# Optimization experiments

Hardware: AMD Instinct MI355X
Metric: run time of the kernel (lower is better)

## Reference

```python
import jax, jax.numpy as jnp
import numpy as np

B, L, C, P, H, DK, MRD = 16, 1024, 512, 64, 8, 64, 7
STD = 0.02


def _layernorm(x, g, b):
    mu = x.mean(-1, keepdims=True)
    var = ((x - mu) ** 2).mean(-1, keepdims=True)
    return (x - mu) / jnp.sqrt(var + 1e-5) * g + b


def _rel_pos_table(L, m):
    i = jnp.arange(L)
    d = jnp.abs(i[:, None] - i[None, :]).astype(jnp.float32)
    d = jnp.where(d > m, m + jnp.log2(jnp.maximum(d - m, 1.0)), d)
    return jnp.clip(d, 0, 2 * m).astype(jnp.int32)  # (L, L) in [0, 2m]


def setup_inputs() -> dict:
    key = jax.random.key(0)
    ks = jax.random.split(key, 16)
    inp = {
        'qx': jax.random.normal(ks[0], (B, L, C), jnp.float32),
        'kx': jax.random.normal(ks[1], (B, L, C), jnp.float32),
        'vx': jax.random.normal(ks[2], (B, L, C), jnp.float32),
        'maskPAD': jnp.ones((B, L, L), jnp.int32),
        'Wp': jax.random.normal(ks[3], (C, P)) * STD,
        'bp': jnp.zeros((P,)),
        'WQ': jax.random.normal(ks[4], (C, H * DK)) * STD,
        'bQ': jnp.zeros((H * DK,)),
        'WK': jax.random.normal(ks[5], (C, H * DK)) * STD,
        'bK': jnp.zeros((H * DK,)),
        'WV': jax.random.normal(ks[6], (C, H * DK)) * STD,
        'bV': jnp.zeros((H * DK,)),
        'WO': jax.random.normal(ks[7], (H * DK, C)) * STD,
        'bO': jnp.zeros((C,)),
        'embK': jax.random.normal(ks[8], (2 * MRD + 1, H)) * STD,
        'embB': jax.random.normal(ks[9], (2 * MRD + 1, H)) * STD,
        'ln1_g': jnp.ones((C,)), 'ln1_b': jnp.zeros((C,)),
        'ln2_g': jnp.ones((C,)), 'ln2_b': jnp.zeros((C,)),
        'W1': jax.random.normal(ks[10], (C, 4 * C)) * STD,
        'b1': jnp.zeros((4 * C,)),
        'W2': jax.random.normal(ks[11], (4 * C, C)) * STD,
        'b2': jnp.zeros((C,)),
    }
    return inp


def reference(qx, kx, vx, maskPAD, Wp, bp, WQ, bQ, WK, bK, WV, bV, WO, bO,
              embK, embB, ln1_g, ln1_b, ln2_g, ln2_b, W1, b1, W2, b2):
    B_, L_, C_ = qx.shape
    P_ = Wp.shape[1]
    H_ = embK.shape[1]
    DK_ = WV.shape[1] // H_
    m = (embK.shape[0] - 1) // 2

    # pseudo-token attention pooling
    pScore = vx @ Wp + bp                                   # (B, L, P)
    pad = (maskPAD[:, 0] == 0)                              # (B, L)
    pScore = jnp.where(pad[:, :, None], -2.0 ** 15, pScore)
    pAlpha = jax.nn.softmax(pScore, axis=1)                 # softmax over L
    kxp = jnp.einsum('blp,blc->bpc', pAlpha, kx)            # (B, P, C)
    vxp = jnp.einsum('blp,blc->bpc', pAlpha, vx)
    pA = jax.lax.stop_gradient(pAlpha)                      # .detach()

    # multi-head attention vs pseudo tokens
    q = (qx @ WQ + bQ).reshape(B_, L_, H_, DK_).transpose(0, 2, 1, 3)   # (B,H,L,dk)
    k = (kxp @ WK + bK).reshape(B_, P_, H_, DK_).transpose(0, 2, 1, 3)  # (B,H,P,dk)
    v = (vxp @ WV + bV).reshape(B_, P_, H_, DK_).transpose(0, 2, 1, 3)
    scores = jnp.einsum('bhld,bhpd->bhlp', q, k) / np.sqrt(DK_).astype(np.float32)

    # relative position multiplicative/additive bias, pooled through pA
    tab = _rel_pos_table(L_, m)                             # (L, L)
    Krel = embK[tab].transpose(2, 0, 1)                     # (H, L, L)
    brel = embB[tab].transpose(2, 0, 1)
    Kb = jnp.einsum('hlm,bmp->bhlp', Krel, pA)
    bb = jnp.einsum('hlm,bmp->bhlp', brel, pA)
    scores = scores * Kb + bb

    alpha = jax.nn.softmax(scores, axis=3)
    z = jnp.einsum('bhlp,bhpd->bhld', alpha, v)
    z = z.transpose(0, 2, 1, 3).reshape(B_, L_, H_ * DK_)
    z = z @ WO + bO

    # FFN block (residuals against vx, post-LN)
    z1 = _layernorm(vx + z, ln1_g, ln1_b)
    ffn = jax.nn.gelu(z1 @ W1 + b1, approximate=False) @ W2 + b2
    x = _layernorm(z1 + ffn, ln2_g, ln2_b)
    return x
```

## Files before the change

### kernel.cpp

```cpp
#include <hip/hip_runtime.h>
#include <hip/hip_bf16.h>

#define BI   16
#define LSEQ 1024
#define CDIM 512
#define PDIM 64
#define HH   8
#define DKK  64

typedef __hip_bfloat16 bf16;
typedef unsigned short u16;
typedef __attribute__((ext_vector_type(8))) short bf16x8;
typedef __attribute__((ext_vector_type(4))) float f32x4;

__constant__ int c_dlo[15] = {0,1,2,3,4,5,6,7, 9,11,15,23,39, 71,135};
__constant__ int c_dhi[15] = {0,1,2,3,4,5,6,8,10,14,22,38,70,134,1023};

__device__ __forceinline__ float b2f(u16 u) {
    union { unsigned int i; float f; } c; c.i = ((unsigned int)u) << 16; return c.f;
}
__device__ __forceinline__ u16 f2bu(float v) {
    bf16 h = __float2bfloat16(v);
    return *(u16*)&h;
}
__device__ __forceinline__ float ldDyn(const void* p, size_t i, int f) {
    return f ? ((const float*)p)[i] : b2f(((const u16*)p)[i]);
}
__device__ __forceinline__ void ld4Dyn(const void* p, size_t i, int f, float* o) {
    if (f) { float4 v = *(const float4*)((const float*)p + i);
             o[0]=v.x; o[1]=v.y; o[2]=v.z; o[3]=v.w; }
    else   { ushort4 u = *(const ushort4*)((const u16*)p + i);
             o[0]=b2f(u.x); o[1]=b2f(u.y); o[2]=b2f(u.z); o[3]=b2f(u.w); }
}

__device__ __forceinline__ void gll16(const u16* g, u16* l) {
    __builtin_amdgcn_global_load_lds(
        (const __attribute__((address_space(1))) unsigned int*)g,
        (__attribute__((address_space(3))) unsigned int*)l,
        16, 0, 0);
}

__device__ __forceinline__ float wsum(float v) {
    #pragma unroll
    for (int o = 32; o; o >>= 1) v += __shfl_xor(v, o, 64);
    return v;
}
__device__ __forceinline__ float wmax(float v) {
    #pragma unroll
    for (int o = 32; o; o >>= 1) v = fmaxf(v, __shfl_xor(v, o, 64));
    return v;
}

__global__ void k_detect(const unsigned int* __restrict__ qw, int* __restrict__ flag) {
    __shared__ int cnt;
    if (threadIdx.x == 0) cnt = 0;
    __syncthreads();
    int local = 0;
    for (int i = threadIdx.x; i < 4096; i += 256) {
        float fv = b2f((u16)(qw[i] & 0xFFFFu));
        float af = fabsf(fv);
        if (fv == 0.0f || (af >= 0.0009765625f && af <= 32.0f)) local++;
    }
    atomicAdd(&cnt, local);
    __syncthreads();
    if (threadIdx.x == 0) flag[0] = (cnt >= 2048) ? 0 : 1;
}

__global__ __launch_bounds__(256) void k_cvt2(
    const void* __restrict__ s0, u16* __restrict__ d0,
    const void* __restrict__ s1, u16* __restrict__ d1,
    const int* __restrict__ flag, int n)
{
    const int fA = flag[0];
    const void* src = blockIdx.y ? s1 : s0;
    u16* dst = blockIdx.y ? d1 : d0;
    int i = (blockIdx.x * 256 + threadIdx.x) * 4;
    if (i >= n) return;
    float t[4]; ld4Dyn(src, i, fA, t);
    ushort4 o; o.x = f2bu(t[0]); o.y = f2bu(t[1]); o.z = f2bu(t[2]); o.w = f2bu(t[3]);
    *(ushort4*)(dst + i) = o;
}

__device__ __forceinline__ void transp_core(
    const void* W, u16* WT, int fd, int Kd, int Nd, int bx, int by)
{
    __shared__ u16 t[32][33];
    const int tx = threadIdx.x & 31, ty = threadIdx.x >> 5;
    #pragma unroll
    for (int r = 0; r < 32; r += 8) {
        int k = by * 32 + ty + r, n = bx * 32 + tx;
        t[ty + r][tx] = f2bu(ldDyn(W, (size_t)k * Nd + n, fd));
    }
    __syncthreads();
    #pragma unroll
    for (int r = 0; r < 32; r += 8) {
        int n = bx * 32 + ty + r, k = by * 32 + tx;
        WT[(size_t)n * Kd + k] = t[tx][ty + r];
    }
}

__global__ __launch_bounds__(256) void k_transp(
    const void* __restrict__ W, u16* __restrict__ WT, const int* __restrict__ flag,
    int Kd, int Nd)
{
    transp_core(W, WT, flag[0], Kd, Nd, blockIdx.x, blockIdx.y);
}

__global__ __launch_bounds__(256) void k_transp4(
    const void* __restrict__ W0, u16* __restrict__ T0,
    const void* __restrict__ W1, u16* __restrict__ T1,
    const void* __restrict__ W2, u16* __restrict__ T2,
    const void* __restrict__ W3, u16* __restrict__ T3,
    const int* __restrict__ flag)
{
    const void* W; u16* T;
    switch (blockIdx.z) {
        case 0: W = W0; T = T0; break;
        case 1: W = W1; T = T1; break;
        case 2: W = W2; T = T2; break;
        default: W = W3; T = T3; break;
    }
    transp_core(W, T, flag[0], 512, 512, blockIdx.x, blockIdx.y);
}

__global__ __launch_bounds__(256) void k_transpcv(
    const void* __restrict__ kx, const u16* __restrict__ vxb,
    u16* __restrict__ kxT, u16* __restrict__ vxT, const int* __restrict__ flag)
{
    const int t = blockIdx.z >> 4;
    const int b = blockIdx.z & 15;
    const int l0 = blockIdx.x * 64, c0 = blockIdx.y * 32;
    __shared__ u16 s[32][72];
    const int tid = threadIdx.x;
    if (t == 0) {
        const int fd = flag[0];
        #pragma unroll
        for (int p = 0; p < 2; ++p) {
            int l = (tid >> 3) + p * 32, c4 = (tid & 7) * 4;
            float v[4];
            ld4Dyn(kx, ((size_t)b * LSEQ + l0 + l) * CDIM + c0 + c4, fd, v);
            #pragma unroll
            for (int k = 0; k < 4; ++k) s[c4 + k][l] = f2bu(v[k]);
        }
    } else {
        #pragma unroll
        for (int p = 0; p < 2; ++p) {
            int l = (tid >> 3) + p * 32, c4 = (tid & 7) * 4;
            ushort4 u = *(const ushort4*)&vxb[((size_t)b * LSEQ + l0 + l) * CDIM + c0 + c4];
            s[c4 + 0][l] = u.x; s[c4 + 1][l] = u.y;
            s[c4 + 2][l] = u.z; s[c4 + 3][l] = u.w;
        }
    }
    __syncthreads();
    u16* dst = t ? vxT : kxT;
    #pragma unroll
    for (int p = 0; p < 2; ++p) {
        int c = (tid >> 4) + p * 16, l4 = (tid & 15) * 4;
        *(ushort4*)&dst[((size_t)b * CDIM + c0 + c) * LSEQ + l0 + l4] =
            *(const ushort4*)&s[c][l4];
    }
}

__device__ __forceinline__ void gemm_core(
    u16 (*As)[32], u16 (*Bs)[32],
    const u16* A, const u16* BT, const void* bias, const u16* res, void* Cc, int fd,
    int K, int lda, int ldbt, int ldc, size_t bOff, int mode, int outBf, int perm,
    int m0, int n0)
{
    const int tid = threadIdx.x;
    const int wave = tid >> 6, lane = tid & 63;
    const int q = lane >> 4, l16 = lane & 15;
    const int wm = (wave >> 1) * 64, wn = (wave & 1) * 64;
    const int srow = wave * 16 + (lane >> 2);
    const int scol = (lane & 3) * 8;

    f32x4 acc[4][4];
    #pragma unroll
    for (int i = 0; i < 4; ++i)
        #pragma unroll
        for (int j = 0; j < 4; ++j) acc[i][j] = (f32x4){0.f, 0.f, 0.f, 0.f};

    #pragma unroll
    for (int pass = 0; pass < 2; ++pass) {
        int row = pass * 64 + srow;
        gll16(A + (size_t)(m0 + row) * lda + scol, &As[pass * 64 + wave * 16][0]);
        gll16(BT + (size_t)(n0 + row) * ldbt + scol, &Bs[pass * 64 + wave * 16][0]);
    }
    __syncthreads();

    int cur = 0;
    for (int k0 = 0; k0 < K; k0 += 32) {
        if (k0 + 32 < K) {
            const int nb = (cur ^ 1) * 128;
            #pragma unroll
            for (int pass = 0; pass < 2; ++pass) {
                int row = pass * 64 + srow;
                gll16(A + (size_t)(m0 + row) * lda + (k0 + 32) + scol,
                      &As[nb + pass * 64 + wave * 16][0]);
                gll16(BT + (size_t)(n0 + row) * ldbt + (k0 + 32) + scol,
                      &Bs[nb + pass * 64 + wave * 16][0]);
            }
        }
        const int cb = cur * 128;
        bf16x8 af[4], bfr[4];
        #pragma unroll
        for (int i = 0; i < 4; ++i) af[i] = *(const bf16x8*)&As[cb + wm + i * 16 + l16][q * 8];
        #pragma unroll
        for (int j = 0; j < 4; ++j) bfr[j] = *(const bf16x8*)&Bs[cb + wn + j * 16 + l16][q * 8];
        #pragma unroll
        for (int i = 0; i < 4; ++i)
            #pragma unroll
            for (int j = 0; j < 4; ++j)
                acc[i][j] = __builtin_amdgcn_mfma_f32_16x16x32_bf16(af[i], bfr[j], acc[i][j], 0, 0, 0);
        __syncthreads();
        cur ^= 1;
    }

    #pragma unroll
    for (int i = 0; i < 4; ++i) {
        int row = m0 + wm + i * 16 + q * 4;
        #pragma unroll
        for (int j = 0; j < 4; ++j) {
            int col = n0 + wn + j * 16 + l16;
            #pragma unroll
            for (int r = 0; r < 4; ++r) {
                float v = acc[i][j][r];
                int m = row + r;
                if (mode == 2) {
                    v += ldDyn(bias, bOff + col, fd) + b2f(res[(size_t)m * ldc + col]);
                    ((float*)Cc)[(size_t)m * ldc + col] = v;
                } else {
                    v += ldDyn(bias, bOff + col, fd);
                    if (mode == 1) v = 0.5f * v * (1.0f + erff(v * 0.70710678118654752f));
                    size_t idx = perm ? (size_t)((m >> 6) << 15) + ((size_t)col << 6) + (m & 63)
                                      : (size_t)m * ldc + col;
                    if (outBf) ((u16*)Cc)[idx] = f2bu(v);
                    else       ((float*)Cc)[idx] = v;
                }
            }
        }
    }
}

__global__ __launch_bounds__(256) void gemm_mfma(
    const u16* __restrict__ A, const u16* __restrict__ BT, const void* __restrict__ bias,
    const u16* __restrict__ res, void* __restrict__ Cc, const int* __restrict__ flag,
    int K, int lda, int ldbt, int ldc, size_t bOff, int mode, int outBf, int perm)
{
    __shared__ u16 As[256][32];
    __shared__ u16 Bs[256][32];
    gemm_core(As, Bs, A, BT, bias, res, Cc, flag[0], K, lda, ldbt, ldc, bOff,
              mode, outBf, perm, blockIdx.y * 128, blockIdx.x * 128);
}

__global__ __launch_bounds__(256) void gemm_kv(
    const u16* __restrict__ A0, const u16* __restrict__ A1,
    const u16* __restrict__ BT0, const u16* __restrict__ BT1,
    const void* __restrict__ b0, const void* __restrict__ b1,
    void* __restrict__ C0, void* __restrict__ C1, const int* __restrict__ flag)
{
    __shared__ u16 As[256][32];
    __shared__ u16 Bs[256][32];
    const int z = blockIdx.z;
    gemm_core(As, Bs, z ? A1 : A0, z ? BT1 : BT0, z ? b1 : b0, nullptr,
              z ? C1 : C0, flag[0],
              CDIM, CDIM, CDIM, CDIM, 0, 0, 1, z ? 1 : 0,
              blockIdx.y * 128, blockIdx.x * 128);
}

__global__ __launch_bounds__(256) void gemm_pool(
    const u16* __restrict__ pAT, const u16* __restrict__ kxT,
    const u16* __restrict__ vxT, u16* __restrict__ kvxb)
{
    __shared__ u16 As[128][32];
    __shared__ u16 Bs[256][32];
    const int b = blockIdx.y;
    const int n0 = blockIdx.x * 128;
    const u16* Ag = pAT + (size_t)b * (PDIM * LSEQ);
    const u16* Bg = (blockIdx.z ? vxT : kxT) + (size_t)b * (CDIM * LSEQ);
    u16* Cg = kvxb + (size_t)blockIdx.z * 524288 + (size_t)b * (PDIM * CDIM);

    const int tid = threadIdx.x;
    const int wave = tid >> 6, lane = tid & 63;
    const int q = lane >> 4, l16 = lane & 15;
    const int wm = (wave >> 1) * 32, wn = (wave & 1) * 64;
    const int srow = lane >> 2, scol = (lane & 3) * 8;

    f32x4 acc[2][4];
    #pragma unroll
    for (int i = 0; i < 2; ++i)
        #pragma unroll
        for (int j = 0; j < 4; ++j) acc[i][j] = (f32x4){0.f, 0.f, 0.f, 0.f};

    gll16(Ag + (size_t)(wave * 16 + srow) * LSEQ + scol, &As[wave * 16][0]);
    #pragma unroll
    for (int pass = 0; pass < 2; ++pass)
        gll16(Bg + (size_t)(n0 + wave * 32 + pass * 16 + srow) * LSEQ + scol,
              &Bs[wave * 32 + pass * 16][0]);
    __syncthreads();

    int cur = 0;
    for (int k0 = 0; k0 < LSEQ; k0 += 32) {
        if (k0 + 32 < LSEQ) {
            const int na = (cur ^ 1) * 64, nb = (cur ^ 1) * 128;
            gll16(Ag + (size_t)(wave * 16 + srow) * LSEQ + (k0 + 32) + scol,
                  &As[na + wave * 16][0]);
            #pragma unroll
            for (int pass = 0; pass < 2; ++pass)
                gll16(Bg + (size_t)(n0 + wave * 32 + pass * 16 + srow) * LSEQ + (k0 + 32) + scol,
                      &Bs[nb + wave * 32 + pass * 16][0]);
        }
        const int ca = cur * 64, cb = cur * 128;
        bf16x8 af[2], bfr[4];
        #pragma unroll
        for (int i = 0; i < 2; ++i) af[i] = *(const bf16x8*)&As[ca + wm + i * 16 + l16][q * 8];
        #pragma unroll
        for (int j = 0; j < 4; ++j) bfr[j] = *(const bf16x8*)&Bs[cb + wn + j * 16 + l16][q * 8];
        #pragma unroll
        for (int i = 0; i < 2; ++i)
            #pragma unroll
            for (int j = 0; j < 4; ++j)
                acc[i][j] = __builtin_amdgcn_mfma_f32_16x16x32_bf16(af[i], bfr[j], acc[i][j], 0, 0, 0);
        __syncthreads();
        cur ^= 1;
    }

    #pragma unroll
    for (int i = 0; i < 2; ++i) {
        int row = wm + i * 16 + q * 4;
        #pragma unroll
        for (int j = 0; j < 4; ++j) {
            int col = n0 + wn + j * 16 + l16;
            #pragma unroll
            for (int r = 0; r < 4; ++r)
                Cg[(size_t)(row + r) * CDIM + col] = f2bu(acc[i][j][r]);
        }
    }
}

__global__ __launch_bounds__(256) void gemm_mfma64(
    const u16* __restrict__ A, const u16* __restrict__ BT, const void* __restrict__ bias,
    float* __restrict__ Cc, const int* __restrict__ flag,
    int K, int lda, int ldbt)
{
    const int fd = flag[0];
    __shared__ u16 As[256][32];
    __shared__ u16 Bs[128][32];
    const int m0 = blockIdx.y * 128;
    const int tid = threadIdx.x;
    const int wave = tid >> 6, lane = tid & 63;
    const int q = lane >> 4, l16 = lane & 15;
    const int wm = wave * 32;
    const int srow = wave * 16 + (lane >> 2);
    const int scol = (lane & 3) * 8;

    f32x4 acc[2][4];
    #pragma unroll
    for (int i = 0; i < 2; ++i)
        #pragma unroll
        for (int j = 0; j < 4; ++j) acc[i][j] = (f32x4){0.f, 0.f, 0.f, 0.f};

    #pragma unroll
    for (int pass = 0; pass < 2; ++pass) {
        int row = pass * 64 + srow;
        gll16(A + (size_t)(m0 + row) * lda + scol, &As[pass * 64 + wave * 16][0]);
    }
    gll16(BT + (size_t)srow * ldbt + scol, &Bs[wave * 16][0]);
    __syncthreads();

    int cur = 0;
    for (int k0 = 0; k0 < K; k0 += 32) {
        if (k0 + 32 < K) {
            const int na = (cur ^ 1) * 128, nb = (cur ^ 1) * 64;
            #pragma unroll
            for (int pass = 0; pass < 2; ++pass) {
                int row = pass * 64 + srow;
                gll16(A + (size_t)(m0 + row) * lda + (k0 + 32) + scol,
                      &As[na + pass * 64 + wave * 16][0]);
            }
            gll16(BT + (size_t)srow * ldbt + (k0 + 32) + scol, &Bs[nb + wave * 16][0]);
        }
        const int ca = cur * 128, cb = cur * 64;
        bf16x8 af[2], bfr[4];
        #pragma unroll
        for (int i = 0; i < 2; ++i) af[i] = *(const bf16x8*)&As[ca + wm + i * 16 + l16][q * 8];
        #pragma unroll
        for (int j = 0; j < 4; ++j) bfr[j] = *(const bf16x8*)&Bs[cb + j * 16 + l16][q * 8];
        #pragma unroll
        for (int i = 0; i < 2; ++i)
            #pragma unroll
            for (int j = 0; j < 4; ++j)
                acc[i][j] = __builtin_amdgcn_mfma_f32_16x16x32_bf16(af[i], bfr[j], acc[i][j], 0, 0, 0);
        __syncthreads();
        cur ^= 1;
    }

    #pragma unroll
    for (int i = 0; i < 2; ++i) {
        int row = m0 + wm + i * 16 + q * 4;
        #pragma unroll
        for (int j = 0; j < 4; ++j) {
            int col = j * 16 + l16;
            #pragma unroll
            for (int r = 0; r < 4; ++r)
                Cc[(size_t)(row + r) * 64 + col] = acc[i][j][r] + ldDyn(bias, col, fd);
        }
    }
}

__global__ __launch_bounds__(256) void gemm_att(
    const u16* __restrict__ Abase, const u16* __restrict__ Bbase,
    void* __restrict__ outp, int mode)
{
    __shared__ u16 Aq[2][128][32];
    __shared__ u16 Bk[2][64][32];
    const int bh = blockIdx.y;
    const int b = bh >> 3, h = bh & 7;
    const int m0 = blockIdx.x * 128;
    const int tid = threadIdx.x;
    const int wave = tid >> 6, lane = tid & 63;
    const int q = lane >> 4, l16 = lane & 15;

    const u16* Ag; const u16* Bg; int lda, ldb;
    if (mode == 0) {
        Ag = Abase + ((size_t)b * LSEQ + m0) * CDIM + h * 64;  lda = CDIM;
        Bg = Bbase + (size_t)b * 32768 + h * 64;               ldb = CDIM;
    } else {
        Ag = Abase + ((size_t)bh * LSEQ + m0) * 64;            lda = 64;
        Bg = Bbase + (size_t)b * 32768 + (size_t)h * 64 * 64;  ldb = 64;
    }

    const int srow = lane >> 2;
    const int scol = (lane & 3) * 8;
    #pragma unroll
    for (int half = 0; half < 2; ++half) {
        #pragma unroll
        for (int pass = 0; pass < 2; ++pass) {
            int row = pass * 64 + wave * 16 + srow;
            gll16(Ag + (size_t)row * lda + half * 32 + scol,
                  &Aq[half][pass * 64 + wave * 16][0]);
        }
        gll16(Bg + (size_t)(wave * 16 + srow) * ldb + half * 32 + scol,
              &Bk[half][wave * 16][0]);
    }
    __syncthreads();

    f32x4 acc[2][4];
    #pragma unroll
    for (int i = 0; i < 2; ++i)
        #pragma unroll
        for (int j = 0; j < 4; ++j) acc[i][j] = (f32x4){0.f, 0.f, 0.f, 0.f};

    #pragma unroll
    for (int kk = 0; kk < 2; ++kk) {
        bf16x8 af[2], bfr[4];
        #pragma unroll
        for (int i = 0; i < 2; ++i)
            af[i] = *(const bf16x8*)&Aq[kk][wave * 32 + i * 16 + l16][q * 8];
        #pragma unroll
        for (int j = 0; j < 4; ++j)
            bfr[j] = *(const bf16x8*)&Bk[kk][j * 16 + l16][q * 8];
        #pragma unroll
        for (int i = 0; i < 2; ++i)
            #pragma unroll
            for (int j = 0; j < 4; ++j)
                acc[i][j] = __builtin_amdgcn_mfma_f32_16x16x32_bf16(af[i], bfr[j], acc[i][j], 0, 0, 0);
    }

    #pragma unroll
    for (int i = 0; i < 2; ++i) {
        int row = m0 + wave * 32 + i * 16 + q * 4;
        #pragma unroll
        for (int j = 0; j < 4; ++j) {
            int col = j * 16 + l16;
            #pragma unroll
            for (int r = 0; r < 4; ++r) {
                if (mode == 0) {
                    ((float*)outp)[((size_t)bh * LSEQ + row + r) * 64 + col] =
                        0.125f * acc[i][j][r];
                } else {
                    ((u16*)outp)[((size_t)b * LSEQ + row + r) * CDIM + h * 64 + col] =
                        f2bu(acc[i][j][r]);
                }
            }
        }
    }
}

__global__ __launch_bounds__(256) void k_softscan(
    const float* __restrict__ psc, const int* __restrict__ maskPAD,
    u16* __restrict__ pAT, float* __restrict__ cumT)
{
    const int b = blockIdx.x >> 6;
    const int p = blockIdx.x & 63;
    const int tid = threadIdx.x;
    __shared__ float s0[1024], s1[1024];
    __shared__ float redA[4], redB[4];

    float acc[4];
    #pragma unroll
    for (int r = 0; r < 4; ++r) {
        int m = tid + r * 256;
        float a = psc[((size_t)b * LSEQ + m) * PDIM + p];
        if (maskPAD[(size_t)b * LSEQ * LSEQ + m] == 0) a = -32768.0f;
        acc[r] = a;
    }
    float mx = fmaxf(fmaxf(acc[0], acc[1]), fmaxf(acc[2], acc[3]));
    mx = wmax(mx);
    if ((tid & 63) == 0) redA[tid >> 6] = mx;
    __syncthreads();
    mx = fmaxf(fmaxf(redA[0], redA[1]), fmaxf(redA[2], redA[3]));

    float e[4], ls = 0.f;
    #pragma unroll
    for (int r = 0; r < 4; ++r) { e[r] = expf(acc[r] - mx); ls += e[r]; }
    ls = wsum(ls);
    if ((tid & 63) == 0) redB[tid >> 6] = ls;
    __syncthreads();
    float inv = 1.0f / (redB[0] + redB[1] + redB[2] + redB[3]);

    #pragma unroll
    for (int r = 0; r < 4; ++r) {
        int m = tid + r * 256;
        float pa = e[r] * inv;
        pAT[((size_t)b * PDIM + p) * LSEQ + m] = f2bu(pa);
        s0[m] = pa;
    }
    __syncthreads();

    float* src = s0; float* dst = s1;
    for (int off = 1; off < 1024; off <<= 1) {
        #pragma unroll
        for (int r = 0; r < 4; ++r) {
            int i = tid + r * 256;
            float v = src[i];
            if (i >= off) v += src[i - off];
            dst[i] = v;
        }
        __syncthreads();
        float* t = src; src = dst; dst = t;
    }
    size_t cb = (size_t)b * (LSEQ + 1) * PDIM + p;
    if (tid == 0) cumT[cb] = 0.f;
    #pragma unroll
    for (int r = 0; r < 4; ++r) {
        int i = tid + r * 256;
        cumT[cb + (size_t)(i + 1) * PDIM] = src[i];
    }
}

__global__ __launch_bounds__(512) void k_sm(
    const float* __restrict__ raw, u16* __restrict__ alb,
    const float* __restrict__ cumT,
    const void* __restrict__ embK, const void* __restrict__ embB,
    const int* __restrict__ flag)
{
    const int fd = flag[0];
    const int b = blockIdx.x >> 10;
    const int l = blockIdx.x & 1023;
    const int tid = threadIdx.x;
    __shared__ float S[15][PDIM];
    __shared__ float eK[120], eB[120];

    if (tid < 120) { eK[tid] = ldDyn(embK, tid, fd); eB[tid] = ldDyn(embB, tid, fd); }

    const float* cb = cumT + (size_t)b * (LSEQ + 1) * PDIM;
    for (int idx = tid; idx < 960; idx += 512) {
        int t = idx >> 6, pp = idx & 63;
        float s;
        if (t == 0) {
            s = cb[(size_t)(l + 1) * 64 + pp] - cb[(size_t)l * 64 + pp];
        } else {
            s = 0.f;
            int hi = l - c_dlo[t];
            int lo = l - c_dhi[t]; if (lo < 0) lo = 0;
            if (hi >= lo) s += cb[(size_t)(hi + 1) * 64 + pp] - cb[(size_t)lo * 64 + pp];
            lo = l + c_dlo[t];
            hi = l + c_dhi[t]; if (hi > 1023) hi = 1023;
            if (lo <= hi) s += cb[(size_t)(hi + 1) * 64 + pp] - cb[(size_t)lo * 64 + pp];
        }
        S[t][pp] = s;
    }
    __syncthreads();

    const int h = tid >> 6, p = tid & 63;
    float kbm = 0.f, bbm = 0.f;
    #pragma unroll
    for (int t = 0; t < 15; ++t) {
        float sv = S[t][p];
        kbm += eK[t * 8 + h] * sv;
        bbm += eB[t * 8 + h] * sv;
    }
    size_t idx = (((size_t)b * 8 + h) * LSEQ + l) * 64 + p;
    float sc = raw[idx] * kbm + bbm;
    float mx = wmax(sc);
    float e  = expf(sc - mx);
    float ssum = wsum(e);
    alb[idx] = f2bu(e / ssum);
}

__global__ __launch_bounds__(512) void k_ln(
    const void* __restrict__ a, const u16* __restrict__ badd,
    const void* __restrict__ g, const void* __restrict__ be, const int* __restrict__ flag,
    void* __restrict__ out, float* __restrict__ out2, const void* __restrict__ bias2,
    int aKind, int outKind)
{
    const int fd = flag[0];
    const int fA = (aKind == 2) ? fd : aKind;
    const int fO = (outKind == 2) ? fd : outKind;
    const size_t row = blockIdx.x;
    const int c = threadIdx.x;
    float x = ldDyn(a, row * CDIM + c, fA);
    if (badd) x += b2f(badd[row * CDIM + c]);

    __shared__ float rA[8], rB[8];
    float s = wsum(x);
    if ((c & 63) == 0) rA[c >> 6] = s;
    __syncthreads();
    float tot = 0.f;
    #pragma unroll
    for (int w = 0; w < 8; ++w) tot += rA[w];
    float mu = tot * (1.0f / 512.0f);
    float dv = x - mu;
    float s2 = wsum(dv * dv);
    if ((c & 63) == 0) rB[c >> 6] = s2;
    __syncthreads();
    float v2 = 0.f;
    #pragma unroll
    for (int w = 0; w < 8; ++w) v2 += rB[w];
    float y = dv * rsqrtf(v2 * (1.0f / 512.0f) + 1e-5f) * ldDyn(g, c, fd) + ldDyn(be, c, fd);
    if (fO) ((float*)out)[row * CDIM + c] = y;
    else    ((u16*)out)[row * CDIM + c] = f2bu(y);
    if (out2) out2[row * CDIM + c] = y + ldDyn(bias2, c, fd);
}

extern "C" void kernel_launch(void* const* d_in, const int* in_sizes, int n_in,
                              void* d_out, int out_size, void* d_ws, size_t ws_size,
                              hipStream_t stream)
{
    (void)in_sizes; (void)n_in; (void)out_size; (void)ws_size;
    const void* qx   = d_in[0];
    const void* kx   = d_in[1];
    const void* vx   = d_in[2];
    const int*  mask = (const int*)d_in[3];
    const void* Wp   = d_in[4];
    const void* bp   = d_in[5];
    const void* WQ   = d_in[6];
    const void* bQ   = d_in[7];
    const void* WK   = d_in[8];
    const void* bK   = d_in[9];
    const void* WV   = d_in[10];
    const void* bV   = d_in[11];
    const void* WO   = d_in[12];
    const void* bO   = d_in[13];
    const void* embK = d_in[14];
    const void* embB = d_in[15];
    const void* l1g  = d_in[16];
    const void* l1b  = d_in[17];
    const void* l2g  = d_in[18];
    const void* l2b  = d_in[19];
    const void* W1   = d_in[20];
    const void* b1   = d_in[21];
    const void* W2   = d_in[22];
    const void* b2   = d_in[23];

    float* ws     = (float*)d_ws;
    int*   flag   = (int*)d_ws;
    float* outF   = ws + 64;
    float* psc    = ws + 64;
    float* cumT   = ws + 1048640;
    u16*   pAT    = (u16*)(ws + 2098240);
    u16*   kbh    = (u16*)(ws + 2622528);
    u16*   vbT    = (u16*)(ws + 2884672);
    u16*   albuf  = (u16*)(ws + 3146816);
    u16*   kvxb   = (u16*)(ws + 7341120);
    u16*   qz     = (u16*)(ws + 8388672);
    u16*   hidden = (u16*)(ws + 12582976);
    u16*   qxb    = hidden;
    u16*   zo     = qxb;
    u16*   vxb    = (u16*)(ws + 16777280);
    u16*   kxT    = (u16*)(ws + 20971584);
    u16*   vxT    = (u16*)(ws + 25165888);
    float* rawbuf = ws + 20971584;
    u16*   WqT    = (u16*)(ws + 29360192);
    u16*   WkT    = (u16*)(ws + 29491264);
    u16*   WvT    = (u16*)(ws + 29622336);
    u16*   WoT    = (u16*)(ws + 29753408);
    u16*   W1T    = (u16*)(ws + 29884480);
    u16*   W2T    = (u16*)(ws + 30408768);
    u16*   WpT    = (u16*)(ws + 30933056);

    const int MROW = BI * LSEQ;

    k_detect<<<dim3(1), dim3(256), 0, stream>>>((const unsigned int*)qx, flag);
    k_cvt2<<<dim3(MROW * CDIM / 1024, 2), dim3(256), 0, stream>>>(
        qx, qxb, vx, vxb, flag, MROW * CDIM);
    k_transp4<<<dim3(16, 16, 4), dim3(256), 0, stream>>>(
        WQ, WqT, WK, WkT, WV, WvT, WO, WoT, flag);
    k_transp<<<dim3(2, 16),  dim3(256), 0, stream>>>(Wp, WpT, flag, 512, 64);
    k_transp<<<dim3(64, 16), dim3(256), 0, stream>>>(W1, W1T, flag, 512, 2048);
    k_transp<<<dim3(16, 64), dim3(256), 0, stream>>>(W2, W2T, flag, 2048, 512);
    k_transpcv<<<dim3(16, 16, 32), dim3(256), 0, stream>>>(kx, vxb, kxT, vxT, flag);

    gemm_mfma64<<<dim3(1, MROW / 128), dim3(256), 0, stream>>>(
        vxb, WpT, bp, psc, flag, CDIM, CDIM, CDIM);
    k_softscan<<<dim3(BI * PDIM), dim3(256), 0, stream>>>(psc, mask, pAT, cumT);
    gemm_pool<<<dim3(4, 16, 2), dim3(256), 0, stream>>>(pAT, kxT, vxT, kvxb);
    gemm_mfma<<<dim3(4, MROW / 128), dim3(256), 0, stream>>>(
        qxb, WqT, bQ, nullptr, qz, flag, CDIM, CDIM, CDIM, CDIM, 0, 0, 1, 0);
    gemm_kv<<<dim3(4, 8, 2), dim3(256), 0, stream>>>(
        kvxb, kvxb + 524288, WkT, WvT, bK, bV, kbh, vbT, flag);
    gemm_att<<<dim3(8, BI * HH), dim3(256), 0, stream>>>(qz, kbh, rawbuf, 0);
    k_sm<<<dim3(BI * LSEQ), dim3(512), 0, stream>>>(
        rawbuf, albuf, cumT, embK, embB, flag);
    gemm_att<<<dim3(8, BI * HH), dim3(256), 0, stream>>>(albuf, vbT, qz, 1);
    gemm_mfma<<<dim3(4, MROW / 128), dim3(256), 0, stream>>>(
        qz, WoT, bO, nullptr, zo, flag, CDIM, CDIM, CDIM, CDIM, 0, 0, 1, 0);
    k_ln<<<dim3(MROW), dim3(512), 0, stream>>>(
        vx, zo, l1g, l1b, flag, qz, nullptr, nullptr, 2, 0);
    gemm_mfma<<<dim3(16, MROW / 128), dim3(256), 0, stream>>>(
        qz, W1T, b1, nullptr, hidden, flag, CDIM, CDIM, CDIM, 2048, 0, 1, 1, 0);
    gemm_mfma<<<dim3(4, MROW / 128), dim3(256), 0, stream>>>(
        hidden, W2T, b2, qz, outF, flag, 2048, 2048, 2048, CDIM, 0, 2, 0, 0);
    k_ln<<<dim3(MROW), dim3(512), 0, stream>>>(
        outF, nullptr, l2g, l2b, flag, d_out, nullptr, nullptr, 1, 2);
}
```

Measured before the change: 682.8 us.

## Triple-buffer GEMM LDS staging and remap workgroups across XCDs

The shared GEMM core moves from a double-buffered K loop with full __syncthreads to a three-stage ring. Loads are issued two tiles ahead, and explicit vmcnt/lgkmcnt waits plus raw s_barrier replace the syncs, so more global-load latency overlaps with MFMA work. gemm_mfma also permutes its linear block index so that consecutive chunks of tiles land on the same XCD, which is meant to improve L2 reuse. LDS use per block grows by half, which may lower occupancy. The hand-counted vmcnt thresholds assume exactly four outstanding loads per stage, and the remap assumes the grid size is divisible by 8.

Measured after the change: 648.3 us. 5.0% less time.

```diff
diff --git a/kernel.cpp b/kernel.cpp
--- a/kernel.cpp
+++ b/kernel.cpp
@@ -173,6 +173,7 @@
     const int wm = (wave >> 1) * 64, wn = (wave & 1) * 64;
     const int srow = wave * 16 + (lane >> 2);
     const int scol = (lane & 3) * 8;
+    const int nt = K >> 5;
 
     f32x4 acc[4][4];
     #pragma unroll
@@ -180,28 +181,30 @@
         #pragma unroll
         for (int j = 0; j < 4; ++j) acc[i][j] = (f32x4){0.f, 0.f, 0.f, 0.f};
 
-    #pragma unroll
-    for (int pass = 0; pass < 2; ++pass) {
-        int row = pass * 64 + srow;
-        gll16(A + (size_t)(m0 + row) * lda + scol, &As[pass * 64 + wave * 16][0]);
-        gll16(BT + (size_t)(n0 + row) * ldbt + scol, &Bs[pass * 64 + wave * 16][0]);
-    }
-    __syncthreads();
-
-    int cur = 0;
-    for (int k0 = 0; k0 < K; k0 += 32) {
-        if (k0 + 32 < K) {
-            const int nb = (cur ^ 1) * 128;
-            #pragma unroll
-            for (int pass = 0; pass < 2; ++pass) {
-                int row = pass * 64 + srow;
-                gll16(A + (size_t)(m0 + row) * lda + (k0 + 32) + scol,
-                      &As[nb + pass * 64 + wave * 16][0]);
-                gll16(BT + (size_t)(n0 + row) * ldbt + (k0 + 32) + scol,
-                      &Bs[nb + pass * 64 + wave * 16][0]);
-            }
-        }
-        const int cb = cur * 128;
+    auto stage = [&](int t, int buf) {
+        const int o = buf * 128;
+        #pragma unroll
+        for (int pass = 0; pass < 2; ++pass) {
+            int row = pass * 64 + srow;
+            gll16(A + (size_t)(m0 + row) * lda + t * 32 + scol,
+                  &As[o + pass * 64 + wave * 16][0]);
+            gll16(BT + (size_t)(n0 + row) * ldbt + t * 32 + scol,
+                  &Bs[o + pass * 64 + wave * 16][0]);
+        }
+    };
+
+    stage(0, 0);
+    if (nt > 1) stage(1, 1);
+
+    for (int t = 0; t < nt; ++t) {
+        if (t + 2 < nt) stage(t + 2, (t + 2) % 3);
+        if (t + 2 < nt)      asm volatile("s_waitcnt vmcnt(8)" ::: "memory");
+        else if (t + 1 < nt) asm volatile("s_waitcnt vmcnt(4)" ::: "memory");
+        else                 asm volatile("s_waitcnt vmcnt(0)" ::: "memory");
+        __builtin_amdgcn_sched_barrier(0);
+        __builtin_amdgcn_s_barrier();
+
+        const int cb = (t % 3) * 128;
         bf16x8 af[4], bfr[4];
         #pragma unroll
         for (int i = 0; i < 4; ++i) af[i] = *(const bf16x8*)&As[cb + wm + i * 16 + l16][q * 8];
@@ -212,8 +215,12 @@
             #pragma unroll
             for (int j = 0; j < 4; ++j)
                 acc[i][j] = __builtin_amdgcn_mfma_f32_16x16x32_bf16(af[i], bfr[j], acc[i][j], 0, 0, 0);
-        __syncthreads();
-        cur ^= 1;
+
+        if (t + 1 < nt) {
+            asm volatile("s_waitcnt lgkmcnt(0)" ::: "memory");
+            __builtin_amdgcn_sched_barrier(0);
+            __builtin_amdgcn_s_barrier();
+        }
     }
 
     #pragma unroll
@@ -247,10 +254,14 @@
     const u16* __restrict__ res, void* __restrict__ Cc, const int* __restrict__ flag,
     int K, int lda, int ldbt, int ldc, size_t bOff, int mode, int outBf, int perm)
 {
-    __shared__ u16 As[256][32];
-    __shared__ u16 Bs[256][32];
+    __shared__ u16 As[384][32];
+    __shared__ u16 Bs[384][32];
+    const int lin = blockIdx.y * gridDim.x + blockIdx.x;
+    const int chunk = (gridDim.x * gridDim.y) >> 3;
+    const int wg = (lin & 7) * chunk + (lin >> 3);
+    const int bx = wg % gridDim.x, by = wg / gridDim.x;
     gemm_core(As, Bs, A, BT, bias, res, Cc, flag[0], K, lda, ldbt, ldc, bOff,
-              mode, outBf, perm, blockIdx.y * 128, blockIdx.x * 128);
+              mode, outBf, perm, by * 128, bx * 128);
 }
 
 __global__ __launch_bounds__(256) void gemm_kv(
@@ -259,8 +270,8 @@
     const void* __restrict__ b0, const void* __restrict__ b1,
     void* __restrict__ C0, void* __restrict__ C1, const int* __restrict__ flag)
 {
-    __shared__ u16 As[256][32];
-    __shared__ u16 Bs[256][32];
+    __shared__ u16 As[384][32];
+    __shared__ u16 Bs[384][32];
     const int z = blockIdx.z;
     gemm_core(As, Bs, z ? A1 : A0, z ? BT1 : BT0, z ? b1 : b0, nullptr,
               z ? C1 : C0, flag[0],
```
